# Optimization experiments

Measured on AMD Instinct MI355X. Metric: run time of the kernel, lower is better.

Reference implementation:

```python
import jax, jax.numpy as jnp
import numpy as np

DIM, EMBED, HEADS = 768, 512, 8
HEAD_DIM = EMBED // HEADS


def setup_inputs() -> dict:
    key = jax.random.key(0)
    ks = jax.random.split(key, 11)
    B, S = 4, 2048
    s = 0.02
    return {
        "query": jax.random.normal(ks[0], (B, S, DIM), jnp.float32),
        "key": jax.random.normal(ks[1], (B, S, DIM), jnp.float32),
        "value": jax.random.normal(ks[2], (B, S, DIM), jnp.float32),
        "wq": jax.random.normal(ks[3], (DIM, EMBED), jnp.float32) * s,
        "bq": jnp.zeros((EMBED,), jnp.float32),
        "wk": jax.random.normal(ks[4], (DIM, EMBED), jnp.float32) * s,
        "bk": jnp.zeros((EMBED,), jnp.float32),
        "wv": jax.random.normal(ks[5], (DIM, EMBED), jnp.float32) * s,
        "bv": jnp.zeros((EMBED,), jnp.float32),
        "wo": jax.random.normal(ks[6], (EMBED, DIM), jnp.float32) * s,
        "bo": jnp.zeros((DIM,), jnp.float32),
    }


def reference(query, key, value, wq, bq, wk, bk, wv, bv, wo, bo):
    B, S, _ = query.shape
    # QKV projections -> [B, H, S, Dh]
    def split_heads(x):
        return x.reshape(B, -1, HEADS, HEAD_DIM).transpose(0, 2, 1, 3)
    q = split_heads(query @ wq + bq)
    k = split_heads(key @ wk + bk)
    v = split_heads(value @ wv + bv)
    scores = jnp.einsum("bhqd,bhkd->bhqk", q, k) / jnp.sqrt(jnp.float32(HEAD_DIM))
    p = jax.nn.softmax(scores, axis=-1)
    x = jnp.einsum("bhqk,bhkd->bhqd", p, v)
    x = x.transpose(0, 2, 1, 3).reshape(B, S, EMBED)
    return x @ wo + bo
```

## Files before the change

### kernel.cpp

```cpp
#include <hip/hip_runtime.h>
#include <math.h>

#define NH   8
#define HD   64
#define BS   4
#define SEQL 2048
#define DIMX 768
#define EMB  512
#define MROWS (BS*SEQL)

typedef __attribute__((ext_vector_type(4))) float          f32x4;
typedef __attribute__((ext_vector_type(8))) __bf16         bf16x8;
typedef __attribute__((ext_vector_type(8))) unsigned short u16x8;
typedef __attribute__((ext_vector_type(4))) unsigned short u16x4;

__device__ __forceinline__ unsigned short f2bf(float x) {
    unsigned int u = __float_as_uint(x);
    u += 0x7FFFu + ((u >> 16) & 1u);
    return (unsigned short)(u >> 16);
}

__global__ __launch_bounds__(256)
void transpose_w4(const float* __restrict__ w0, const float* __restrict__ w1,
                  const float* __restrict__ w2, const float* __restrict__ w3,
                  unsigned short* __restrict__ o0, unsigned short* __restrict__ o1,
                  unsigned short* __restrict__ o2, unsigned short* __restrict__ o3)
{
    __shared__ float sm[32][33];
    const int which = blockIdx.y;
    const float* in; unsigned short* out; int R, C;
    if      (which == 0) { in = w0; out = o0; R = DIMX; C = EMB;  }
    else if (which == 1) { in = w1; out = o1; R = DIMX; C = EMB;  }
    else if (which == 2) { in = w2; out = o2; R = DIMX; C = EMB;  }
    else                 { in = w3; out = o3; R = EMB;  C = DIMX; }
    const int nbx = C / 32;
    const int rB = (blockIdx.x / nbx) * 32, cB = (blockIdx.x % nbx) * 32;
    const int row = threadIdx.x >> 3, c4 = (threadIdx.x & 7) * 4;
    f32x4 v = *(const f32x4*)&in[(size_t)(rB + row) * C + cB + c4];
    sm[row][c4 + 0] = v[0]; sm[row][c4 + 1] = v[1];
    sm[row][c4 + 2] = v[2]; sm[row][c4 + 3] = v[3];
    __syncthreads();
    u16x4 o;
    o[0] = f2bf(sm[c4 + 0][row]); o[1] = f2bf(sm[c4 + 1][row]);
    o[2] = f2bf(sm[c4 + 2][row]); o[3] = f2bf(sm[c4 + 3][row]);
    *(u16x4*)&out[(size_t)(cB + row) * R + rB + c4] = o;
}

__global__ __launch_bounds__(256)
void transpose_v(const unsigned short* __restrict__ Vb, unsigned short* __restrict__ Vt) {
    __shared__ unsigned short sm[64][72];
    const int sBase = blockIdx.x * 64;
    const int bh = blockIdx.y;
    const int b = bh >> 3, h = bh & 7;
    const unsigned short* inb = Vb + (size_t)(b * SEQL + sBase) * EMB + h * HD;
    #pragma unroll
    for (int p = 0; p < 2; ++p) {
        int c = threadIdx.x + p * 256;
        int row = c >> 3, c8 = (c & 7) * 8;
        u16x8 v = *(const u16x8*)&inb[(size_t)row * EMB + c8];
        *(u16x8*)&sm[row][c8] = v;
    }
    __syncthreads();
    const int d = threadIdx.x >> 2, s0 = (threadIdx.x & 3) * 16;
    u16x8 o0, o1;
    #pragma unroll
    for (int j = 0; j < 8; ++j) { o0[j] = sm[s0 + j][d]; o1[j] = sm[s0 + 8 + j][d]; }
    unsigned short* ob = Vt + (size_t)(bh * HD + d) * SEQL + sBase + s0;
    *(u16x8*)&ob[0] = o0;
    *(u16x8*)&ob[8] = o1;
}

template<bool AFP32>
__global__ __launch_bounds__(256)
void gemm_bt(const void* __restrict__ Av, const unsigned short* __restrict__ Bt,
             const float* __restrict__ bias, float* __restrict__ Cf,
             unsigned short* __restrict__ Cb, int K, int N, int mode, float oscale)
{
    __shared__ unsigned short smA[128 * 72];
    __shared__ unsigned short smB[64 * 72];
    const int tid = threadIdx.x;
    const int w = tid >> 6, lane = tid & 63;
    const int quad = lane >> 4, lanem = lane & 15;
    const int wm = w >> 1, wn = w & 1;
    const int mBase = blockIdx.y * 128, nBase = blockIdx.x * 64;

    const f32x4 z4 = {0.f, 0.f, 0.f, 0.f};
    f32x4 acc[4][2];
    #pragma unroll
    for (int mt = 0; mt < 4; ++mt)
        #pragma unroll
        for (int nt = 0; nt < 2; ++nt) acc[mt][nt] = z4;

    for (int k0 = 0; k0 < K; k0 += 64) {
        u16x8 va[4], vb[2];
        #pragma unroll
        for (int p = 0; p < 4; ++p) {
            int c = tid + p * 256;
            int row = c >> 3, c8 = (c & 7) * 8;
            if constexpr (AFP32) {
                const float* Af = (const float*)Av;
                f32x4 x0 = *(const f32x4*)&Af[(size_t)(mBase + row) * K + k0 + c8];
                f32x4 x1 = *(const f32x4*)&Af[(size_t)(mBase + row) * K + k0 + c8 + 4];
                u16x8 t;
                t[0] = f2bf(x0[0]); t[1] = f2bf(x0[1]); t[2] = f2bf(x0[2]); t[3] = f2bf(x0[3]);
                t[4] = f2bf(x1[0]); t[5] = f2bf(x1[1]); t[6] = f2bf(x1[2]); t[7] = f2bf(x1[3]);
                va[p] = t;
            } else {
                const unsigned short* Ab = (const unsigned short*)Av;
                va[p] = *(const u16x8*)&Ab[(size_t)(mBase + row) * K + k0 + c8];
            }
        }
        #pragma unroll
        for (int p = 0; p < 2; ++p) {
            int c = tid + p * 256;
            int row = c >> 3, c8 = (c & 7) * 8;
            vb[p] = *(const u16x8*)&Bt[(size_t)(nBase + row) * K + k0 + c8];
        }
        __syncthreads();
        #pragma unroll
        for (int p = 0; p < 4; ++p) {
            int c = tid + p * 256;
            *(u16x8*)&smA[(c >> 3) * 72 + (c & 7) * 8] = va[p];
        }
        #pragma unroll
        for (int p = 0; p < 2; ++p) {
            int c = tid + p * 256;
            *(u16x8*)&smB[(c >> 3) * 72 + (c & 7) * 8] = vb[p];
        }
        __syncthreads();
        #pragma unroll
        for (int kk = 0; kk < 64; kk += 32) {
            bf16x8 a[4], bf[2];
            #pragma unroll
            for (int mt = 0; mt < 4; ++mt)
                a[mt] = *(const bf16x8*)&smA[(wm * 64 + mt * 16 + lanem) * 72 + kk + quad * 8];
            #pragma unroll
            for (int nt = 0; nt < 2; ++nt)
                bf[nt] = *(const bf16x8*)&smB[(wn * 32 + nt * 16 + lanem) * 72 + kk + quad * 8];
            #pragma unroll
            for (int mt = 0; mt < 4; ++mt)
                #pragma unroll
                for (int nt = 0; nt < 2; ++nt)
                    acc[mt][nt] = __builtin_amdgcn_mfma_f32_16x16x32_bf16(a[mt], bf[nt], acc[mt][nt], 0, 0, 0);
        }
    }

    #pragma unroll
    for (int mt = 0; mt < 4; ++mt) {
        #pragma unroll
        for (int nt = 0; nt < 2; ++nt) {
            const int n = nBase + wn * 32 + nt * 16 + lanem;
            const float bv = bias[n];
            #pragma unroll
            for (int r = 0; r < 4; ++r) {
                const int m = mBase + wm * 64 + mt * 16 + quad * 4 + r;
                const float val = acc[mt][nt][r] + bv;
                if (mode == 0) Cf[(size_t)m * N + n] = val;
                else           Cb[(size_t)m * N + n] = f2bf(val * oscale);
            }
        }
    }
}

__global__ __launch_bounds__(256)
void attn_mfma(const unsigned short* __restrict__ Qb, const unsigned short* __restrict__ Kb,
               const unsigned short* __restrict__ Vt, unsigned short* __restrict__ Xb)
{
    __shared__ unsigned short smK[64 * 72];
    __shared__ unsigned short smV[64 * 72];
    __shared__ unsigned short smP[4][32 * 72];
    const int tid = threadIdx.x;
    const int w = tid >> 6, lane = tid & 63;
    const int quad = lane >> 4, lanem = lane & 15;
    const int qBase = blockIdx.x * 128;
    const int bh = blockIdx.y;
    const int b = bh >> 3, h = bh & 7;

    bf16x8 aq[2][2];
    #pragma unroll
    for (int rg = 0; rg < 2; ++rg) {
        const size_t qrow = (size_t)(b * SEQL + qBase + w * 32 + rg * 16 + lanem) * EMB + h * HD;
        aq[rg][0] = *(const bf16x8*)&Qb[qrow + quad * 8];
        aq[rg][1] = *(const bf16x8*)&Qb[qrow + 32 + quad * 8];
    }

    const f32x4 z4 = {0.f, 0.f, 0.f, 0.f};
    f32x4 o[4][2];
    float l[2] = {0.f, 0.f};
    #pragma unroll
    for (int dt = 0; dt < 4; ++dt)
        #pragma unroll
        for (int rg = 0; rg < 2; ++rg) o[dt][rg] = z4;

    const unsigned short* Kbase = Kb + (size_t)b * SEQL * EMB + h * HD;
    const unsigned short* Vbase = Vt + (size_t)bh * HD * SEQL;
    unsigned short* pW = &smP[w][0];

    for (int k0 = 0; k0 < SEQL; k0 += 64) {
        u16x8 kv[2], vv[2];
        #pragma unroll
        for (int p = 0; p < 2; ++p) {
            int c = tid + p * 256;
            int row = c >> 3, c8 = (c & 7) * 8;
            kv[p] = *(const u16x8*)&Kbase[(size_t)(k0 + row) * EMB + c8];
            vv[p] = *(const u16x8*)&Vbase[(size_t)row * SEQL + k0 + c8];
        }
        __syncthreads();
        #pragma unroll
        for (int p = 0; p < 2; ++p) {
            int c = tid + p * 256;
            int row = c >> 3, c8 = (c & 7) * 8;
            *(u16x8*)&smK[row * 72 + c8] = kv[p];
            *(u16x8*)&smV[row * 72 + c8] = vv[p];
        }
        __syncthreads();

        #pragma unroll
        for (int nt = 0; nt < 4; ++nt) {
            bf16x8 bk0 = *(const bf16x8*)&smK[(nt * 16 + lanem) * 72 + quad * 8];
            bf16x8 bk1 = *(const bf16x8*)&smK[(nt * 16 + lanem) * 72 + 32 + quad * 8];
            #pragma unroll
            for (int rg = 0; rg < 2; ++rg) {
                f32x4 s = __builtin_amdgcn_mfma_f32_16x16x32_bf16(bk0, aq[rg][0], z4, 0, 0, 0);
                s = __builtin_amdgcn_mfma_f32_16x16x32_bf16(bk1, aq[rg][1], s, 0, 0, 0);
                u16x4 pk;
                #pragma unroll
                for (int r = 0; r < 4; ++r) {
                    float pv = __expf(s[r]);
                    l[rg] += pv;
                    pk[r] = f2bf(pv);
                }
                *(u16x4*)&pW[(rg * 16 + lanem) * 72 + nt * 16 + quad * 4] = pk;
            }
        }
        bf16x8 pb[2][2];
        #pragma unroll
        for (int rg = 0; rg < 2; ++rg) {
            pb[rg][0] = *(const bf16x8*)&pW[(rg * 16 + lanem) * 72 + quad * 8];
            pb[rg][1] = *(const bf16x8*)&pW[(rg * 16 + lanem) * 72 + 32 + quad * 8];
        }
        #pragma unroll
        for (int dt = 0; dt < 4; ++dt) {
            bf16x8 av0 = *(const bf16x8*)&smV[(dt * 16 + lanem) * 72 + quad * 8];
            bf16x8 av1 = *(const bf16x8*)&smV[(dt * 16 + lanem) * 72 + 32 + quad * 8];
            #pragma unroll
            for (int rg = 0; rg < 2; ++rg) {
                o[dt][rg] = __builtin_amdgcn_mfma_f32_16x16x32_bf16(av0, pb[rg][0], o[dt][rg], 0, 0, 0);
                o[dt][rg] = __builtin_amdgcn_mfma_f32_16x16x32_bf16(av1, pb[rg][1], o[dt][rg], 0, 0, 0);
            }
        }
    }

    #pragma unroll
    for (int rg = 0; rg < 2; ++rg) {
        float s = l[rg];
        s += __shfl_xor(s, 16, 64);
        s += __shfl_xor(s, 32, 64);
        l[rg] = 1.f / s;
    }
    #pragma unroll
    for (int rg = 0; rg < 2; ++rg) {
        const size_t orow = (size_t)(b * SEQL + qBase + w * 32 + rg * 16 + lanem) * EMB + h * HD;
        #pragma unroll
        for (int dt = 0; dt < 4; ++dt) {
            u16x4 ov;
            #pragma unroll
            for (int r = 0; r < 4; ++r) ov[r] = f2bf(o[dt][rg][r] * l[rg]);
            *(u16x4*)&Xb[orow + dt * 16 + quad * 4] = ov;
        }
    }
}

extern "C" void kernel_launch(void* const* d_in, const int* in_sizes, int n_in,
                              void* d_out, int out_size, void* d_ws, size_t ws_size,
                              hipStream_t stream) {
    (void)in_sizes; (void)n_in; (void)out_size; (void)ws_size;
    const float* query = (const float*)d_in[0];
    const float* key   = (const float*)d_in[1];
    const float* value = (const float*)d_in[2];
    const float* wq = (const float*)d_in[3];
    const float* bq = (const float*)d_in[4];
    const float* wk = (const float*)d_in[5];
    const float* bk = (const float*)d_in[6];
    const float* wv = (const float*)d_in[7];
    const float* bv = (const float*)d_in[8];
    const float* wo = (const float*)d_in[9];
    const float* bo = (const float*)d_in[10];
    float* out = (float*)d_out;

    char* ws = (char*)d_ws;
    unsigned short* Wqt  = (unsigned short*)(ws);
    unsigned short* Wkt  = (unsigned short*)(ws + 786432);
    unsigned short* Wvt  = (unsigned short*)(ws + 1572864);
    unsigned short* Wot  = (unsigned short*)(ws + 2359296);
    unsigned short* Qbuf = (unsigned short*)(ws + 3145728);
    unsigned short* Kbuf = (unsigned short*)(ws + 11534336);
    unsigned short* Vbuf = (unsigned short*)(ws + 19922944);
    unsigned short* Vtb  = (unsigned short*)(ws + 28311552);
    unsigned short* Xbuf = (unsigned short*)(ws + 36700160);

    const dim3 blk(256);

    transpose_w4<<<dim3(384, 4), blk, 0, stream>>>(wq, wk, wv, wo, Wqt, Wkt, Wvt, Wot);

    gemm_bt<true><<<dim3(EMB / 64, MROWS / 128), blk, 0, stream>>>(query, Wqt, bq, nullptr, Qbuf, DIMX, EMB, 1, 0.125f);
    gemm_bt<true><<<dim3(EMB / 64, MROWS / 128), blk, 0, stream>>>(key,   Wkt, bk, nullptr, Kbuf, DIMX, EMB, 1, 1.0f);
    gemm_bt<true><<<dim3(EMB / 64, MROWS / 128), blk, 0, stream>>>(value, Wvt, bv, nullptr, Vbuf, DIMX, EMB, 1, 1.0f);
    transpose_v<<<dim3(SEQL / 64, BS * NH), blk, 0, stream>>>(Vbuf, Vtb);

    attn_mfma<<<dim3(SEQL / 128, BS * NH), blk, 0, stream>>>(Qbuf, Kbuf, Vtb, Xbuf);

    gemm_bt<false><<<dim3(DIMX / 64, MROWS / 128), blk, 0, stream>>>(Xbuf, Wot, bo, out, nullptr, EMB, DIMX, 0, 1.0f);
}
```

Measured before the change: 290.5 us.

## Restructure pipeline: pre-cast inputs, fused QKV GEMM, register-prefetched attention

Inputs are first cast to bf16 in a separate kernel. Q, K and V then run as one batched GEMM launch with 128x128 tiles, and the V epilogue writes the transposed layout directly, so the separate V transpose goes away. Attention drops the shared-memory K/V staging and instead prefetches K/V fragments into registers from global memory, and it swaps expf for exp2 with the log2e factor folded into the Q scale. P is truncated to bf16 instead of rounded, and row sums are computed on the matrix cores with a ones vector. Register pressure and uncoalesced per-lane global loads in attention are risks, and the extra cast pass adds memory traffic.

```diff
diff --git a/kernel.cpp b/kernel.cpp
--- a/kernel.cpp
+++ b/kernel.cpp
@@ -14,10 +14,37 @@
 typedef __attribute__((ext_vector_type(8))) unsigned short u16x8;
 typedef __attribute__((ext_vector_type(4))) unsigned short u16x4;
 
+union BF8 { u16x8 u; bf16x8 b; };
+
 __device__ __forceinline__ unsigned short f2bf(float x) {
     unsigned int u = __float_as_uint(x);
     u += 0x7FFFu + ((u >> 16) & 1u);
     return (unsigned short)(u >> 16);
+}
+
+#if __has_builtin(__builtin_amdgcn_exp2f)
+#define EXP2F(x) __builtin_amdgcn_exp2f(x)
+#else
+#define EXP2F(x) exp2f(x)
+#endif
+
+__device__ __forceinline__ bf16x8 ldb8(const unsigned short* p) {
+    return *(const bf16x8*)p;
+}
+
+__global__ __launch_bounds__(256)
+void cast3(const float* __restrict__ q, const float* __restrict__ k,
+           const float* __restrict__ v, unsigned short* __restrict__ out)
+{
+    const float* src = blockIdx.y == 0 ? q : (blockIdx.y == 1 ? k : v);
+    unsigned short* dst = out + (size_t)blockIdx.y * (MROWS * DIMX);
+    const int n4 = MROWS * DIMX / 4;
+    for (int i = blockIdx.x * 256 + threadIdx.x; i < n4; i += gridDim.x * 256) {
+        f32x4 x = ((const f32x4*)src)[i];
+        u16x4 o;
+        o[0] = f2bf(x[0]); o[1] = f2bf(x[1]); o[2] = f2bf(x[2]); o[3] = f2bf(x[3]);
+        ((u16x4*)dst)[i] = o;
+    }
 }
 
 __global__ __launch_bounds__(256)
@@ -46,226 +73,254 @@
     *(u16x4*)&out[(size_t)(cB + row) * R + rB + c4] = o;
 }
 
-__global__ __launch_bounds__(256)
-void transpose_v(const unsigned short* __restrict__ Vb, unsigned short* __restrict__ Vt) {
-    __shared__ unsigned short sm[64][72];
-    const int sBase = blockIdx.x * 64;
-    const int bh = blockIdx.y;
+template<bool DIRECT>
+__device__ __forceinline__ void gemm_core(
+    const unsigned short* __restrict__ A, const unsigned short* __restrict__ Bt,
+    int K, int mBase, int nBase,
+    unsigned short* __restrict__ smA, unsigned short* __restrict__ smB,
+    f32x4 (&acc)[4][4])
+{
+    const int tid = threadIdx.x;
+    const int lane = tid & 63, w = tid >> 6;
+    const int quad = lane >> 4, lanem = lane & 15;
+    const int wm = w >> 1, wn = w & 1;
+    const int srow = tid >> 3, c8 = (tid & 7) * 8;
+
+    const f32x4 z4 = {0.f, 0.f, 0.f, 0.f};
+    #pragma unroll
+    for (int i = 0; i < 4; ++i)
+        #pragma unroll
+        for (int j = 0; j < 4; ++j) acc[i][j] = z4;
+
+    for (int k0 = 0; k0 < K; k0 += 64) {
+        u16x8 va[4], vb[4];
+        #pragma unroll
+        for (int p = 0; p < 4; ++p) {
+            va[p] = *(const u16x8*)&A[(size_t)(mBase + srow + p * 32) * K + k0 + c8];
+            vb[p] = *(const u16x8*)&Bt[(size_t)(nBase + srow + p * 32) * K + k0 + c8];
+        }
+        __syncthreads();
+        #pragma unroll
+        for (int p = 0; p < 4; ++p) {
+            *(u16x8*)&smA[(srow + p * 32) * 72 + c8] = va[p];
+            *(u16x8*)&smB[(srow + p * 32) * 72 + c8] = vb[p];
+        }
+        __syncthreads();
+        #pragma unroll
+        for (int kk = 0; kk < 64; kk += 32) {
+            bf16x8 xa[4], wb[4];
+            #pragma unroll
+            for (int mt = 0; mt < 4; ++mt)
+                xa[mt] = ldb8(&smA[(wm * 64 + mt * 16 + lanem) * 72 + kk + quad * 8]);
+            #pragma unroll
+            for (int nt = 0; nt < 4; ++nt)
+                wb[nt] = ldb8(&smB[(wn * 64 + nt * 16 + lanem) * 72 + kk + quad * 8]);
+            if constexpr (DIRECT) {
+                #pragma unroll
+                for (int mt = 0; mt < 4; ++mt)
+                    #pragma unroll
+                    for (int nt = 0; nt < 4; ++nt)
+                        acc[mt][nt] = __builtin_amdgcn_mfma_f32_16x16x32_bf16(xa[mt], wb[nt], acc[mt][nt], 0, 0, 0);
+            } else {
+                #pragma unroll
+                for (int nt = 0; nt < 4; ++nt)
+                    #pragma unroll
+                    for (int mt = 0; mt < 4; ++mt)
+                        acc[nt][mt] = __builtin_amdgcn_mfma_f32_16x16x32_bf16(wb[nt], xa[mt], acc[nt][mt], 0, 0, 0);
+            }
+        }
+    }
+}
+
+__global__ __launch_bounds__(256)
+void gemm_qkv(const unsigned short* __restrict__ Xc, const unsigned short* __restrict__ Wt,
+              const float* __restrict__ bq, const float* __restrict__ bk,
+              const float* __restrict__ bv,
+              unsigned short* __restrict__ Qb, unsigned short* __restrict__ Kb,
+              unsigned short* __restrict__ Vtb)
+{
+    __shared__ unsigned short smA[128 * 72];
+    __shared__ unsigned short smB[128 * 72];
+    const int z = blockIdx.z;
+    const unsigned short* A  = Xc + (size_t)z * (MROWS * DIMX);
+    const unsigned short* Bt = Wt + (size_t)z * (EMB * DIMX);
+    const float* bias = z == 0 ? bq : (z == 1 ? bk : bv);
+    const int mBase = blockIdx.y * 128, nBase = blockIdx.x * 128;
+
+    const int tid = threadIdx.x;
+    const int lane = tid & 63, w = tid >> 6;
+    const int quad = lane >> 4, lanem = lane & 15;
+    const int wm = w >> 1, wn = w & 1;
+
+    f32x4 acc[4][4];
+    if (z == 2) {
+        gemm_core<true>(A, Bt, DIMX, mBase, nBase, smA, smB, acc);
+        #pragma unroll
+        for (int mt = 0; mt < 4; ++mt) {
+            const int sg = mBase + wm * 64 + mt * 16 + quad * 4;
+            const int b = sg >> 11, s = sg & 2047;
+            #pragma unroll
+            for (int nt = 0; nt < 4; ++nt) {
+                const int de = nBase + wn * 64 + nt * 16 + lanem;
+                const float bvv = bias[de];
+                const int h = de >> 6, dh = de & 63;
+                u16x4 ov;
+                #pragma unroll
+                for (int r = 0; r < 4; ++r) ov[r] = f2bf(acc[mt][nt][r] + bvv);
+                *(u16x4*)&Vtb[((size_t)((b * NH + h) * HD + dh) << 11) + s] = ov;
+            }
+        }
+    } else {
+        gemm_core<false>(A, Bt, DIMX, mBase, nBase, smA, smB, acc);
+        const float os = (z == 0) ? 0.18033688f : 1.0f;
+        unsigned short* C = (z == 0) ? Qb : Kb;
+        #pragma unroll
+        for (int nt = 0; nt < 4; ++nt) {
+            const int n0 = nBase + wn * 64 + nt * 16 + quad * 4;
+            const f32x4 b4 = *(const f32x4*)&bias[n0];
+            #pragma unroll
+            for (int mt = 0; mt < 4; ++mt) {
+                const int m = mBase + wm * 64 + mt * 16 + lanem;
+                u16x4 ov;
+                #pragma unroll
+                for (int r = 0; r < 4; ++r) ov[r] = f2bf((acc[nt][mt][r] + b4[r]) * os);
+                *(u16x4*)&C[(size_t)m * EMB + n0] = ov;
+            }
+        }
+    }
+}
+
+__global__ __launch_bounds__(256)
+void gemm_out(const unsigned short* __restrict__ Xb, const unsigned short* __restrict__ Wot,
+              const float* __restrict__ bo, float* __restrict__ out)
+{
+    __shared__ unsigned short smA[128 * 72];
+    __shared__ unsigned short smB[128 * 72];
+    const int mBase = blockIdx.y * 128, nBase = blockIdx.x * 128;
+    const int tid = threadIdx.x;
+    const int lane = tid & 63, w = tid >> 6;
+    const int quad = lane >> 4, lanem = lane & 15;
+    const int wm = w >> 1, wn = w & 1;
+
+    f32x4 acc[4][4];
+    gemm_core<false>(Xb, Wot, EMB, mBase, nBase, smA, smB, acc);
+    #pragma unroll
+    for (int nt = 0; nt < 4; ++nt) {
+        const int n0 = nBase + wn * 64 + nt * 16 + quad * 4;
+        const f32x4 b4 = *(const f32x4*)&bo[n0];
+        #pragma unroll
+        for (int mt = 0; mt < 4; ++mt) {
+            const int m = mBase + wm * 64 + mt * 16 + lanem;
+            f32x4 ov = acc[nt][mt] + b4;
+            *(f32x4*)&out[(size_t)m * DIMX + n0] = ov;
+        }
+    }
+}
+
+__global__ __launch_bounds__(256)
+void attn_mfma(const unsigned short* __restrict__ Qb, const unsigned short* __restrict__ Kb,
+               const unsigned short* __restrict__ Vt, unsigned short* __restrict__ Xb)
+{
+    __shared__ unsigned short smP[4][32 * 72];
+    const int id = blockIdx.x;
+    const int bh = (id & 7) | (((id >> 3) & 3) << 3);
+    const int qb = id >> 5;
     const int b = bh >> 3, h = bh & 7;
-    const unsigned short* inb = Vb + (size_t)(b * SEQL + sBase) * EMB + h * HD;
-    #pragma unroll
-    for (int p = 0; p < 2; ++p) {
-        int c = threadIdx.x + p * 256;
-        int row = c >> 3, c8 = (c & 7) * 8;
-        u16x8 v = *(const u16x8*)&inb[(size_t)row * EMB + c8];
-        *(u16x8*)&sm[row][c8] = v;
-    }
-    __syncthreads();
-    const int d = threadIdx.x >> 2, s0 = (threadIdx.x & 3) * 16;
-    u16x8 o0, o1;
-    #pragma unroll
-    for (int j = 0; j < 8; ++j) { o0[j] = sm[s0 + j][d]; o1[j] = sm[s0 + 8 + j][d]; }
-    unsigned short* ob = Vt + (size_t)(bh * HD + d) * SEQL + sBase + s0;
-    *(u16x8*)&ob[0] = o0;
-    *(u16x8*)&ob[8] = o1;
-}
-
-template<bool AFP32>
-__global__ __launch_bounds__(256)
-void gemm_bt(const void* __restrict__ Av, const unsigned short* __restrict__ Bt,
-             const float* __restrict__ bias, float* __restrict__ Cf,
-             unsigned short* __restrict__ Cb, int K, int N, int mode, float oscale)
-{
-    __shared__ unsigned short smA[128 * 72];
-    __shared__ unsigned short smB[64 * 72];
+
     const int tid = threadIdx.x;
     const int w = tid >> 6, lane = tid & 63;
     const int quad = lane >> 4, lanem = lane & 15;
-    const int wm = w >> 1, wn = w & 1;
-    const int mBase = blockIdx.y * 128, nBase = blockIdx.x * 64;
-
-    const f32x4 z4 = {0.f, 0.f, 0.f, 0.f};
-    f32x4 acc[4][2];
-    #pragma unroll
-    for (int mt = 0; mt < 4; ++mt)
-        #pragma unroll
-        for (int nt = 0; nt < 2; ++nt) acc[mt][nt] = z4;
-
-    for (int k0 = 0; k0 < K; k0 += 64) {
-        u16x8 va[4], vb[2];
-        #pragma unroll
-        for (int p = 0; p < 4; ++p) {
-            int c = tid + p * 256;
-            int row = c >> 3, c8 = (c & 7) * 8;
-            if constexpr (AFP32) {
-                const float* Af = (const float*)Av;
-                f32x4 x0 = *(const f32x4*)&Af[(size_t)(mBase + row) * K + k0 + c8];
-                f32x4 x1 = *(const f32x4*)&Af[(size_t)(mBase + row) * K + k0 + c8 + 4];
-                u16x8 t;
-                t[0] = f2bf(x0[0]); t[1] = f2bf(x0[1]); t[2] = f2bf(x0[2]); t[3] = f2bf(x0[3]);
-                t[4] = f2bf(x1[0]); t[5] = f2bf(x1[1]); t[6] = f2bf(x1[2]); t[7] = f2bf(x1[3]);
-                va[p] = t;
-            } else {
-                const unsigned short* Ab = (const unsigned short*)Av;
-                va[p] = *(const u16x8*)&Ab[(size_t)(mBase + row) * K + k0 + c8];
-            }
-        }
-        #pragma unroll
-        for (int p = 0; p < 2; ++p) {
-            int c = tid + p * 256;
-            int row = c >> 3, c8 = (c & 7) * 8;
-            vb[p] = *(const u16x8*)&Bt[(size_t)(nBase + row) * K + k0 + c8];
-        }
-        __syncthreads();
-        #pragma unroll
-        for (int p = 0; p < 4; ++p) {
-            int c = tid + p * 256;
-            *(u16x8*)&smA[(c >> 3) * 72 + (c & 7) * 8] = va[p];
-        }
-        #pragma unroll
-        for (int p = 0; p < 2; ++p) {
-            int c = tid + p * 256;
-            *(u16x8*)&smB[(c >> 3) * 72 + (c & 7) * 8] = vb[p];
-        }
-        __syncthreads();
-        #pragma unroll
-        for (int kk = 0; kk < 64; kk += 32) {
-            bf16x8 a[4], bf[2];
-            #pragma unroll
-            for (int mt = 0; mt < 4; ++mt)
-                a[mt] = *(const bf16x8*)&smA[(wm * 64 + mt * 16 + lanem) * 72 + kk + quad * 8];
-            #pragma unroll
-            for (int nt = 0; nt < 2; ++nt)
-                bf[nt] = *(const bf16x8*)&smB[(wn * 32 + nt * 16 + lanem) * 72 + kk + quad * 8];
-            #pragma unroll
-            for (int mt = 0; mt < 4; ++mt)
-                #pragma unroll
-                for (int nt = 0; nt < 2; ++nt)
-                    acc[mt][nt] = __builtin_amdgcn_mfma_f32_16x16x32_bf16(a[mt], bf[nt], acc[mt][nt], 0, 0, 0);
-        }
-    }
-
-    #pragma unroll
-    for (int mt = 0; mt < 4; ++mt) {
-        #pragma unroll
-        for (int nt = 0; nt < 2; ++nt) {
-            const int n = nBase + wn * 32 + nt * 16 + lanem;
-            const float bv = bias[n];
-            #pragma unroll
-            for (int r = 0; r < 4; ++r) {
-                const int m = mBase + wm * 64 + mt * 16 + quad * 4 + r;
-                const float val = acc[mt][nt][r] + bv;
-                if (mode == 0) Cf[(size_t)m * N + n] = val;
-                else           Cb[(size_t)m * N + n] = f2bf(val * oscale);
-            }
-        }
-    }
-}
-
-__global__ __launch_bounds__(256)
-void attn_mfma(const unsigned short* __restrict__ Qb, const unsigned short* __restrict__ Kb,
-               const unsigned short* __restrict__ Vt, unsigned short* __restrict__ Xb)
-{
-    __shared__ unsigned short smK[64 * 72];
-    __shared__ unsigned short smV[64 * 72];
-    __shared__ unsigned short smP[4][32 * 72];
-    const int tid = threadIdx.x;
-    const int w = tid >> 6, lane = tid & 63;
-    const int quad = lane >> 4, lanem = lane & 15;
-    const int qBase = blockIdx.x * 128;
-    const int bh = blockIdx.y;
-    const int b = bh >> 3, h = bh & 7;
 
     bf16x8 aq[2][2];
     #pragma unroll
     for (int rg = 0; rg < 2; ++rg) {
-        const size_t qrow = (size_t)(b * SEQL + qBase + w * 32 + rg * 16 + lanem) * EMB + h * HD;
-        aq[rg][0] = *(const bf16x8*)&Qb[qrow + quad * 8];
-        aq[rg][1] = *(const bf16x8*)&Qb[qrow + 32 + quad * 8];
+        const size_t qrow = (size_t)(b * SEQL + qb * 128 + w * 32 + rg * 16 + lanem) * EMB + h * HD;
+        aq[rg][0] = ldb8(&Qb[qrow + quad * 8]);
+        aq[rg][1] = ldb8(&Qb[qrow + 32 + quad * 8]);
     }
 
     const f32x4 z4 = {0.f, 0.f, 0.f, 0.f};
     f32x4 o[4][2];
-    float l[2] = {0.f, 0.f};
+    f32x4 ls[2] = {z4, z4};
     #pragma unroll
     for (int dt = 0; dt < 4; ++dt)
         #pragma unroll
         for (int rg = 0; rg < 2; ++rg) o[dt][rg] = z4;
+
+    BF8 ones;
+    #pragma unroll
+    for (int i = 0; i < 8; ++i) ones.u[i] = 0x3F80;
 
     const unsigned short* Kbase = Kb + (size_t)b * SEQL * EMB + h * HD;
     const unsigned short* Vbase = Vt + (size_t)bh * HD * SEQL;
     unsigned short* pW = &smP[w][0];
 
+    bf16x8 kf[4][2], vf[4][2];
+    #pragma unroll
+    for (int nt = 0; nt < 4; ++nt)
+        #pragma unroll
+        for (int hf = 0; hf < 2; ++hf) {
+            kf[nt][hf] = ldb8(&Kbase[(size_t)(nt * 16 + lanem) * EMB + hf * 32 + quad * 8]);
+            vf[nt][hf] = ldb8(&Vbase[(size_t)(nt * 16 + lanem) * SEQL + hf * 32 + quad * 8]);
+        }
+
     for (int k0 = 0; k0 < SEQL; k0 += 64) {
-        u16x8 kv[2], vv[2];
-        #pragma unroll
-        for (int p = 0; p < 2; ++p) {
-            int c = tid + p * 256;
-            int row = c >> 3, c8 = (c & 7) * 8;
-            kv[p] = *(const u16x8*)&Kbase[(size_t)(k0 + row) * EMB + c8];
-            vv[p] = *(const u16x8*)&Vbase[(size_t)row * SEQL + k0 + c8];
-        }
-        __syncthreads();
-        #pragma unroll
-        for (int p = 0; p < 2; ++p) {
-            int c = tid + p * 256;
-            int row = c >> 3, c8 = (c & 7) * 8;
-            *(u16x8*)&smK[row * 72 + c8] = kv[p];
-            *(u16x8*)&smV[row * 72 + c8] = vv[p];
-        }
-        __syncthreads();
+        const int kn = (k0 + 64 < SEQL) ? k0 + 64 : 0;
+        bf16x8 kfn[4][2], vfn[4][2];
+        #pragma unroll
+        for (int nt = 0; nt < 4; ++nt)
+            #pragma unroll
+            for (int hf = 0; hf < 2; ++hf) {
+                kfn[nt][hf] = ldb8(&Kbase[(size_t)(kn + nt * 16 + lanem) * EMB + hf * 32 + quad * 8]);
+                vfn[nt][hf] = ldb8(&Vbase[(size_t)(nt * 16 + lanem) * SEQL + kn + hf * 32 + quad * 8]);
+            }
 
         #pragma unroll
         for (int nt = 0; nt < 4; ++nt) {
-            bf16x8 bk0 = *(const bf16x8*)&smK[(nt * 16 + lanem) * 72 + quad * 8];
-            bf16x8 bk1 = *(const bf16x8*)&smK[(nt * 16 + lanem) * 72 + 32 + quad * 8];
             #pragma unroll
             for (int rg = 0; rg < 2; ++rg) {
-                f32x4 s = __builtin_amdgcn_mfma_f32_16x16x32_bf16(bk0, aq[rg][0], z4, 0, 0, 0);
-                s = __builtin_amdgcn_mfma_f32_16x16x32_bf16(bk1, aq[rg][1], s, 0, 0, 0);
+                f32x4 s = __builtin_amdgcn_mfma_f32_16x16x32_bf16(kf[nt][0], aq[rg][0], z4, 0, 0, 0);
+                s = __builtin_amdgcn_mfma_f32_16x16x32_bf16(kf[nt][1], aq[rg][1], s, 0, 0, 0);
                 u16x4 pk;
                 #pragma unroll
-                for (int r = 0; r < 4; ++r) {
-                    float pv = __expf(s[r]);
-                    l[rg] += pv;
-                    pk[r] = f2bf(pv);
-                }
+                for (int r = 0; r < 4; ++r)
+                    pk[r] = (unsigned short)(__float_as_uint(EXP2F(s[r])) >> 16);
                 *(u16x4*)&pW[(rg * 16 + lanem) * 72 + nt * 16 + quad * 4] = pk;
             }
         }
         bf16x8 pb[2][2];
         #pragma unroll
         for (int rg = 0; rg < 2; ++rg) {
-            pb[rg][0] = *(const bf16x8*)&pW[(rg * 16 + lanem) * 72 + quad * 8];
-            pb[rg][1] = *(const bf16x8*)&pW[(rg * 16 + lanem) * 72 + 32 + quad * 8];
-        }
-        #pragma unroll
-        for (int dt = 0; dt < 4; ++dt) {
-            bf16x8 av0 = *(const bf16x8*)&smV[(dt * 16 + lanem) * 72 + quad * 8];
-            bf16x8 av1 = *(const bf16x8*)&smV[(dt * 16 + lanem) * 72 + 32 + quad * 8];
+            pb[rg][0] = ldb8(&pW[(rg * 16 + lanem) * 72 + quad * 8]);
+            pb[rg][1] = ldb8(&pW[(rg * 16 + lanem) * 72 + 32 + quad * 8]);
+        }
+        #pragma unroll
+        for (int dt = 0; dt < 4; ++dt)
             #pragma unroll
             for (int rg = 0; rg < 2; ++rg) {
-                o[dt][rg] = __builtin_amdgcn_mfma_f32_16x16x32_bf16(av0, pb[rg][0], o[dt][rg], 0, 0, 0);
-                o[dt][rg] = __builtin_amdgcn_mfma_f32_16x16x32_bf16(av1, pb[rg][1], o[dt][rg], 0, 0, 0);
-            }
-        }
+                o[dt][rg] = __builtin_amdgcn_mfma_f32_16x16x32_bf16(vf[dt][0], pb[rg][0], o[dt][rg], 0, 0, 0);
+                o[dt][rg] = __builtin_amdgcn_mfma_f32_16x16x32_bf16(vf[dt][1], pb[rg][1], o[dt][rg], 0, 0, 0);
+            }
+        #pragma unroll
+        for (int rg = 0; rg < 2; ++rg) {
+            ls[rg] = __builtin_amdgcn_mfma_f32_16x16x32_bf16(ones.b, pb[rg][0], ls[rg], 0, 0, 0);
+            ls[rg] = __builtin_amdgcn_mfma_f32_16x16x32_bf16(ones.b, pb[rg][1], ls[rg], 0, 0, 0);
+        }
+        #pragma unroll
+        for (int nt = 0; nt < 4; ++nt)
+            #pragma unroll
+            for (int hf = 0; hf < 2; ++hf) { kf[nt][hf] = kfn[nt][hf]; vf[nt][hf] = vfn[nt][hf]; }
     }
 
     #pragma unroll
     for (int rg = 0; rg < 2; ++rg) {
-        float s = l[rg];
-        s += __shfl_xor(s, 16, 64);
-        s += __shfl_xor(s, 32, 64);
-        l[rg] = 1.f / s;
-    }
-    #pragma unroll
-    for (int rg = 0; rg < 2; ++rg) {
-        const size_t orow = (size_t)(b * SEQL + qBase + w * 32 + rg * 16 + lanem) * EMB + h * HD;
+        const float rinv = 1.f / ls[rg][0];
+        const size_t orow = (size_t)(b * SEQL + qb * 128 + w * 32 + rg * 16 + lanem) * EMB + h * HD;
         #pragma unroll
         for (int dt = 0; dt < 4; ++dt) {
             u16x4 ov;
             #pragma unroll
-            for (int r = 0; r < 4; ++r) ov[r] = f2bf(o[dt][rg][r] * l[rg]);
+            for (int r = 0; r < 4; ++r) ov[r] = f2bf(o[dt][rg][r] * rinv);
             *(u16x4*)&Xb[orow + dt * 16 + quad * 4] = ov;
         }
     }
@@ -289,26 +344,24 @@
     float* out = (float*)d_out;
 
     char* ws = (char*)d_ws;
-    unsigned short* Wqt  = (unsigned short*)(ws);
-    unsigned short* Wkt  = (unsigned short*)(ws + 786432);
-    unsigned short* Wvt  = (unsigned short*)(ws + 1572864);
-    unsigned short* Wot  = (unsigned short*)(ws + 2359296);
-    unsigned short* Qbuf = (unsigned short*)(ws + 3145728);
-    unsigned short* Kbuf = (unsigned short*)(ws + 11534336);
-    unsigned short* Vbuf = (unsigned short*)(ws + 19922944);
-    unsigned short* Vtb  = (unsigned short*)(ws + 28311552);
-    unsigned short* Xbuf = (unsigned short*)(ws + 36700160);
+    unsigned short* castb = (unsigned short*)(ws);
+    unsigned short* Xbuf  = (unsigned short*)(ws);
+    unsigned short* Wt    = (unsigned short*)(ws + 37748736);
+    unsigned short* Wot   = (unsigned short*)(ws + 40108032);
+    unsigned short* Qbuf  = (unsigned short*)(ws + 40894464);
+    unsigned short* Kbuf  = (unsigned short*)(ws + 49283072);
+    unsigned short* Vtb   = (unsigned short*)(ws + 57671680);
 
     const dim3 blk(256);
 
-    transpose_w4<<<dim3(384, 4), blk, 0, stream>>>(wq, wk, wv, wo, Wqt, Wkt, Wvt, Wot);
-
-    gemm_bt<true><<<dim3(EMB / 64, MROWS / 128), blk, 0, stream>>>(query, Wqt, bq, nullptr, Qbuf, DIMX, EMB, 1, 0.125f);
-    gemm_bt<true><<<dim3(EMB / 64, MROWS / 128), blk, 0, stream>>>(key,   Wkt, bk, nullptr, Kbuf, DIMX, EMB, 1, 1.0f);
-    gemm_bt<true><<<dim3(EMB / 64, MROWS / 128), blk, 0, stream>>>(value, Wvt, bv, nullptr, Vbuf, DIMX, EMB, 1, 1.0f);
-    transpose_v<<<dim3(SEQL / 64, BS * NH), blk, 0, stream>>>(Vbuf, Vtb);
-
-    attn_mfma<<<dim3(SEQL / 128, BS * NH), blk, 0, stream>>>(Qbuf, Kbuf, Vtb, Xbuf);
-
-    gemm_bt<false><<<dim3(DIMX / 64, MROWS / 128), blk, 0, stream>>>(Xbuf, Wot, bo, out, nullptr, EMB, DIMX, 0, 1.0f);
-}
+    transpose_w4<<<dim3(384, 4), blk, 0, stream>>>(wq, wk, wv, wo,
+        Wt, Wt + (size_t)EMB * DIMX, Wt + 2 * (size_t)EMB * DIMX, Wot);
+    cast3<<<dim3(1024, 3), blk, 0, stream>>>(query, key, value, castb);
+
+    gemm_qkv<<<dim3(EMB / 128, MROWS / 128, 3), blk, 0, stream>>>(
+        castb, Wt, bq, bk, bv, Qbuf, Kbuf, Vtb);
+
+    attn_mfma<<<dim3(512), blk, 0, stream>>>(Qbuf, Kbuf, Vtb, Xbuf);
+
+    gemm_out<<<dim3(DIMX / 128, MROWS / 128), blk, 0, stream>>>(Xbuf, Wot, bo, out);
+}
```

Measured after the change: 304.3 us. 4.8% more time.
